# Performance work log

Hardware: AMD Instinct MI355X
Metric: run time of the kernel (lower is better)

The kernel has to match this reference:

```python
import jax, jax.numpy as jnp
import numpy as np


def _conv1x1(x, W, b):
    # x: (n, c_in, h, w); W: (c_out, c_in); b: (c_out,)
    return jnp.einsum('nchw,oc->nohw', x, W) + b[None, :, None, None]


def setup_inputs() -> dict:
    key = jax.random.key(0)
    ks = jax.random.split(key, 9)
    n, C, h, w = 2, 256, 64, 64
    Ch = C // 2
    s_in = 0.02
    return {
        'feature': jax.random.normal(ks[0], (n, C, h, w), dtype=jnp.float32),
        'Wq': jax.random.normal(ks[1], (Ch, C), dtype=jnp.float32) * s_in,
        'bq': jax.random.normal(ks[2], (Ch,), dtype=jnp.float32) * s_in,
        'Wk': jax.random.normal(ks[3], (Ch, C), dtype=jnp.float32) * s_in,
        'bk': jax.random.normal(ks[4], (Ch,), dtype=jnp.float32) * s_in,
        'Wv': jax.random.normal(ks[5], (Ch, C), dtype=jnp.float32) * s_in,
        'bv': jax.random.normal(ks[6], (Ch,), dtype=jnp.float32) * s_in,
        'Wm': jax.random.normal(ks[7], (C, Ch), dtype=jnp.float32) * s_in,
        'bm': jax.random.normal(ks[8], (C,), dtype=jnp.float32) * s_in,
    }


def reference(feature, Wq, bq, Wk, bk, Wv, bv, Wm, bm):
    n, C, h, w = feature.shape
    Ch = C // 2
    N = n * h * w
    # 1x1 conv projections, then flatten batch+spatial into one sequence dim
    q = _conv1x1(feature, Wq, bq)  # (n, Ch, h, w)
    k = _conv1x1(feature, Wk, bk)
    v = _conv1x1(feature, Wv, bv)
    # NCHW -> NHWC -> (N, Ch), matching torch transpose(1,2).transpose(2,3).reshape
    q = jnp.transpose(q, (0, 2, 3, 1)).reshape(N, Ch)
    k = jnp.transpose(k, (0, 2, 3, 1)).reshape(N, Ch)
    v = jnp.transpose(v, (0, 2, 3, 1)).reshape(N, Ch)
    # scores = k @ q.T (note: torch code uses k as rows, q.T as cols)
    scores = k @ q.T  # (N, N)
    attn = jax.nn.softmax(scores, axis=-1)
    mask = attn @ v  # (N, Ch)
    mask = mask.reshape(n, h, w, Ch)
    # torch transpose chain (2,3)->(1,2)->(2,3): (n,h,w,Ch) -> (n,Ch,w,h)
    mask = jnp.transpose(mask, (0, 3, 2, 1))
    out = _conv1x1(mask, Wm, bm)  # (n, C, w, h); h==w so residual add is valid
    return out + feature
```

## Files before the change

kernel.cpp:

```cpp
#include <hip/hip_runtime.h>
#include <hip/hip_bf16.h>

#define LOG2E 1.44269504088896340736f

typedef __attribute__((ext_vector_type(8))) short short8;
typedef __attribute__((ext_vector_type(4))) float f32x4;
typedef __attribute__((ext_vector_type(2))) unsigned int uint2v;
typedef __attribute__((ext_vector_type(4))) unsigned int uint4v;
typedef unsigned int u32;

__device__ __forceinline__ short f2bf(float f) {
    unsigned u = __builtin_bit_cast(unsigned, f);
    unsigned r = (u + 0x7FFFu + ((u >> 16) & 1u)) >> 16;
    return (short)r;
}

__device__ __forceinline__ float bf2f(short x) {
    unsigned u = ((unsigned)(unsigned short)x) << 16;
    return __builtin_bit_cast(float, u);
}

__device__ __forceinline__ unsigned cvt_pk_bf16(float lo, float hi) {
    unsigned r;
    asm volatile("v_cvt_pk_bf16_f32 %0, %1, %2" : "=v"(r) : "v"(lo), "v"(hi));
    return r;
}

__device__ __forceinline__ float fexp2(float x) {
    float r;
    asm("v_exp_f32 %0, %1" : "=v"(r) : "v"(x));
    return r;
}

__global__ __launch_bounds__(64) void wprep_kernel(
    const float* __restrict__ Wq, const float* __restrict__ bq,
    const float* __restrict__ Wk, const float* __restrict__ bk,
    const float* __restrict__ Wv, const float* __restrict__ bv,
    const float* __restrict__ Wm,
    short* __restrict__ Wb, float* __restrict__ bqkv, short* __restrict__ Wmb)
{
    const int b = blockIdx.x;
    const int t = threadIdx.x;
    if (b < 384) {
        const int mat = b >> 7, row = b & 127;
        const float* src = (mat == 0 ? Wq : mat == 1 ? Wk : Wv) + (size_t)row * 256;
        const float sc = (mat == 1) ? LOG2E : 1.f;
        float4 v = *(const float4*)(src + t * 4);
        uint2v pk;
        pk.x = cvt_pk_bf16(v.x * sc, v.y * sc);
        pk.y = cvt_pk_bf16(v.z * sc, v.w * sc);
        *(uint2v*)(Wb + (size_t)b * 256 + t * 4) = pk;
    } else if (b == 384) {
        for (int e = t; e < 384; e += 64) {
            const int mat = e >> 7;
            const float* bsrc = (mat == 0 ? bq : mat == 1 ? bk : bv);
            bqkv[e] = bsrc[e & 127] * (mat == 1 ? LOG2E : 1.f);
        }
    } else {
        const int row = b - 385;
        float2 v = *(const float2*)(Wm + (size_t)row * 128 + t * 2);
        *(u32*)(Wmb + (size_t)row * 128 + t * 2) = cvt_pk_bf16(v.x, v.y);
    }
}

__global__ __launch_bounds__(256) void proj_kernel(
    const float* __restrict__ feat, const short* __restrict__ Wb,
    const float* __restrict__ bqkv,
    short* __restrict__ Qb, short* __restrict__ Kb, short* __restrict__ VTp)
{
    __shared__ __align__(16) short Xs[16 * 256];
    __shared__ __align__(16) short VTs[128 * 16];
    const int t = threadIdx.x;
    const int blk = blockIdx.x;
    const int ib = blk * 16;
    const int n = ib >> 12;
    const int hw0 = ib & 4095;

    {
        const int r = t & 15, cg = t >> 4;
        const float* fp = feat + (size_t)n * 1048576 + (size_t)(cg * 16) * 4096 + hw0 + r;
        short8 t0, t1;
        #pragma unroll
        for (int ci = 0; ci < 8; ++ci) {
            t0[ci] = f2bf(fp[(size_t)ci * 4096]);
            t1[ci] = f2bf(fp[(size_t)(ci + 8) * 4096]);
        }
        const int sw = (r & 7) << 2;
        *(short8*)(&Xs[r * 256 + ((cg * 2) ^ sw) * 8]) = t0;
        *(short8*)(&Xs[r * 256 + ((cg * 2 + 1) ^ sw) * 8]) = t1;
    }
    __syncthreads();

    const int lane = t & 63;
    const int w = __builtin_amdgcn_readfirstlane(t >> 6);
    const int l15 = lane & 15;
    const int g = lane >> 4;
    const int o0w = w * 96;

    f32x4 acc[6];
    #pragma unroll
    for (int osub = 0; osub < 6; ++osub)
        acc[osub] = *(const f32x4*)(bqkv + o0w + osub * 16 + 4 * g);

    const short* wbase = Wb + (size_t)(o0w + l15) * 256 + g * 8;
    const int xsw = (l15 & 7) << 2;
    #pragma unroll
    for (int kc = 0; kc < 8; ++kc) {
        short8 xf = *(const short8*)(&Xs[l15 * 256 + (((kc * 4 + g) ^ xsw) * 8)]);
        #pragma unroll
        for (int osub = 0; osub < 6; ++osub) {
            short8 wf = *(const short8*)(wbase + (size_t)osub * 16 * 256 + kc * 32);
            acc[osub] = __builtin_amdgcn_mfma_f32_16x16x32_bf16(wf, xf, acc[osub], 0, 0, 0);
        }
    }

    #pragma unroll
    for (int osub = 0; osub < 6; ++osub) {
        const int o0 = o0w + osub * 16;
        const int mat = o0 >> 7;
        const int col = (o0 & 127) + 4 * g;
        if (mat == 0) {
            uint2v pk;
            pk.x = cvt_pk_bf16(acc[osub][0], acc[osub][1]);
            pk.y = cvt_pk_bf16(acc[osub][2], acc[osub][3]);
            *(uint2v*)(Qb + (size_t)(ib + l15) * 128 + col) = pk;
        } else if (mat == 1) {
            uint2v pk;
            pk.x = cvt_pk_bf16(acc[osub][0], acc[osub][1]);
            pk.y = cvt_pk_bf16(acc[osub][2], acc[osub][3]);
            *(uint2v*)(Kb + (size_t)(ib + l15) * 128 + col) = pk;
        } else {
            #pragma unroll
            for (int reg = 0; reg < 4; ++reg)
                VTs[(col + reg) * 16 + l15] = f2bf(acc[osub][reg]);
        }
    }
    __syncthreads();

    {
        const int o = t >> 1, ih = (t & 1) * 8;
        short8 vv = *(const short8*)(&VTs[o * 16 + ih]);
        const int base32 = ib & ~31;
        const int u = (ib >> 4) & 1;
        const int p0 = 2 * ih + 4 * u;
        uint4v q = __builtin_bit_cast(uint4v, vv);
        uint2v lo; lo.x = q.x; lo.y = q.y;
        uint2v hi; hi.x = q.z; hi.y = q.w;
        *(uint2v*)(VTp + (size_t)o * 8192 + base32 + p0) = lo;
        *(uint2v*)(VTp + (size_t)o * 8192 + base32 + p0 + 8) = hi;
    }
}

__global__ __launch_bounds__(256, 3) void attn_kernel(
    const short* __restrict__ Qb, const short* __restrict__ Kb,
    const short* __restrict__ VTp,
    short* __restrict__ Opart, float* __restrict__ Ssb)
{
    __shared__ __align__(16) char smem[32768];

    const int tid = threadIdx.x;
    const int lane = tid & 63;
    const int w = __builtin_amdgcn_readfirstlane(tid >> 6);
    const int l15 = lane & 15;
    const int g = lane >> 4;
    const int blk = blockIdx.x;
    const int ibX = blk >> 4;
    const int jq  = blk & 15;
    const int iw  = ibX * 128 + w * 32;
    const int j0  = jq * 512;

    short8 kf[2][4];
    #pragma unroll
    for (int iset = 0; iset < 2; ++iset)
        #pragma unroll
        for (int dcq = 0; dcq < 4; ++dcq)
            kf[iset][dcq] = *(const short8*)(Kb + (size_t)(iw + iset * 16 + l15) * 128 + dcq * 32 + g * 8);

    f32x4 O[2][8];
    #pragma unroll
    for (int iset = 0; iset < 2; ++iset)
        #pragma unroll
        for (int dc = 0; dc < 8; ++dc) O[iset][dc] = (f32x4){0.f, 0.f, 0.f, 0.f};
    float s[2] = {0.f, 0.f};

    auto stage = [&](int tt, int buf) {
        const int jt = j0 + tt * 32;
        char* base = smem + buf * 16384;
        #pragma unroll
        for (int p = 0; p < 4; ++p) {
            const int seg = p * 4 + w;
            const short* src;
            if (seg < 8) {
                int r = 4 * seg + (lane >> 4), c = lane & 15;
                int cs = c ^ (r & 7);
                src = Qb + (size_t)(jt + r) * 128 + cs * 8;
            } else {
                int s8 = seg - 8;
                int d = 16 * s8 + (lane >> 2), c = lane & 3;
                int cs = c ^ (d & 3);
                src = VTp + (size_t)d * 8192 + jt + cs * 8;
            }
            __builtin_amdgcn_global_load_lds(
                (const __attribute__((address_space(1))) u32*)(const void*)src,
                (__attribute__((address_space(3))) u32*)(void*)(base + seg * 1024),
                16, 0, 0);
        }
    };

    auto compute32 = [&](const char* base) {
        const char* Qt = base;
        const char* Vt = base + 8192;
        const int xs = (l15 & 7) << 4;

        f32x4 sv[2][2];
        #pragma unroll
        for (int jh = 0; jh < 2; ++jh)
            #pragma unroll
            for (int iset = 0; iset < 2; ++iset)
                sv[jh][iset] = (f32x4){-16.f, -16.f, -16.f, -16.f};

        __builtin_amdgcn_s_setprio(1);
        #pragma unroll
        for (int dcq = 0; dcq < 4; ++dcq) {
            short8 qa0 = *(const short8*)(Qt + ((l15 * 256 + dcq * 64 + g * 16) ^ xs));
            short8 qa1 = *(const short8*)(Qt + (((l15 + 16) * 256 + dcq * 64 + g * 16) ^ xs));
            sv[0][0] = __builtin_amdgcn_mfma_f32_16x16x32_bf16(qa0, kf[0][dcq], sv[0][0], 0, 0, 0);
            sv[0][1] = __builtin_amdgcn_mfma_f32_16x16x32_bf16(qa0, kf[1][dcq], sv[0][1], 0, 0, 0);
            sv[1][0] = __builtin_amdgcn_mfma_f32_16x16x32_bf16(qa1, kf[0][dcq], sv[1][0], 0, 0, 0);
            sv[1][1] = __builtin_amdgcn_mfma_f32_16x16x32_bf16(qa1, kf[1][dcq], sv[1][1], 0, 0, 0);
        }
        __builtin_amdgcn_s_setprio(0);

        short8 pf[2];
        #pragma unroll
        for (int iset = 0; iset < 2; ++iset) {
            float p0[4], p1[4], ps = 0.f;
            #pragma unroll
            for (int e = 0; e < 4; ++e) {
                p0[e] = fexp2(sv[0][iset][e]);
                p1[e] = fexp2(sv[1][iset][e]);
                ps += p0[e] + p1[e];
            }
            s[iset] += ps;
            uint4v pk;
            pk.x = cvt_pk_bf16(p0[0], p0[1]);
            pk.y = cvt_pk_bf16(p0[2], p0[3]);
            pk.z = cvt_pk_bf16(p1[0], p1[1]);
            pk.w = cvt_pk_bf16(p1[2], p1[3]);
            pf[iset] = __builtin_bit_cast(short8, pk);
        }

        __builtin_amdgcn_s_setprio(1);
        #pragma unroll
        for (int dc = 0; dc < 8; ++dc) {
            short8 va = *(const short8*)(Vt + (dc * 16 + l15) * 64 + ((g ^ (l15 & 3)) << 4));
            O[0][dc] = __builtin_amdgcn_mfma_f32_16x16x32_bf16(va, pf[0], O[0][dc], 0, 0, 0);
            O[1][dc] = __builtin_amdgcn_mfma_f32_16x16x32_bf16(va, pf[1], O[1][dc], 0, 0, 0);
        }
        __builtin_amdgcn_s_setprio(0);
    };

    stage(0, 0);
    __syncthreads();
    int buf = 0;
    for (int tt = 0; tt < 16; ++tt) {
        if (tt + 1 < 16) stage(tt + 1, buf ^ 1);
        compute32(smem + buf * 16384);
        __syncthreads();
        buf ^= 1;
    }

    #pragma unroll
    for (int iset = 0; iset < 2; ++iset) {
        const int i = iw + iset * 16 + l15;
        #pragma unroll
        for (int dc = 0; dc < 8; ++dc) {
            uint2v pk;
            pk.x = cvt_pk_bf16(O[iset][dc][0], O[iset][dc][1]);
            pk.y = cvt_pk_bf16(O[iset][dc][2], O[iset][dc][3]);
            *(uint2v*)(Opart + (size_t)(jq * 8192 + i) * 128 + dc * 16 + 4 * g) = pk;
        }
        Ssb[(((size_t)jq * 8192 + i) << 2) + g] = s[iset];
    }
}

__global__ __launch_bounds__(256) void merge_kernel(
    const short* __restrict__ Opart, const float* __restrict__ Ssb,
    short* __restrict__ maskbb)
{
    const int t = threadIdx.x, b = blockIdx.x;
    const int row = b * 32 + (t >> 3);
    const int d0 = (t & 7) * 16;

    float T = 0.f;
    #pragma unroll
    for (int q = 0; q < 16; ++q) {
        f32x4 s4 = *(const f32x4*)(Ssb + (((size_t)q * 8192 + row) << 2));
        T += (s4[0] + s4[1]) + (s4[2] + s4[3]);
    }

    float acc[16];
    #pragma unroll
    for (int e = 0; e < 16; ++e) acc[e] = 0.f;
    #pragma unroll
    for (int q = 0; q < 16; ++q) {
        const short* op = Opart + (size_t)(q * 8192 + row) * 128 + d0;
        short8 o0 = *(const short8*)(op);
        short8 o1 = *(const short8*)(op + 8);
        #pragma unroll
        for (int e = 0; e < 8; ++e) {
            acc[e]     += bf2f(o0[e]);
            acc[8 + e] += bf2f(o1[e]);
        }
    }
    const float inv = 1.f / T;
    uint4v pk0, pk1;
    pk0.x = cvt_pk_bf16(acc[0] * inv, acc[1] * inv);
    pk0.y = cvt_pk_bf16(acc[2] * inv, acc[3] * inv);
    pk0.z = cvt_pk_bf16(acc[4] * inv, acc[5] * inv);
    pk0.w = cvt_pk_bf16(acc[6] * inv, acc[7] * inv);
    pk1.x = cvt_pk_bf16(acc[8] * inv, acc[9] * inv);
    pk1.y = cvt_pk_bf16(acc[10] * inv, acc[11] * inv);
    pk1.z = cvt_pk_bf16(acc[12] * inv, acc[13] * inv);
    pk1.w = cvt_pk_bf16(acc[14] * inv, acc[15] * inv);
    short* mp = maskbb + (size_t)row * 128 + d0;
    *(uint4v*)(mp) = pk0;
    *(uint4v*)(mp + 8) = pk1;
}

__global__ __launch_bounds__(256, 4) void epi_kernel(
    const short* __restrict__ maskbb, const short* __restrict__ Wmb,
    const float* __restrict__ bm, const float* __restrict__ feat,
    float* __restrict__ out)
{
    __shared__ __align__(16) short Ms[16 * 128];
    const int t = threadIdx.x;
    const int blk = blockIdx.x;
    const int yt = blk & 3;
    const int x = (blk >> 2) & 63;
    const int n = blk >> 8;
    const int y0 = yt * 16;

    {
        const int r = t >> 4, c = t & 15;
        const int i = n * 4096 + (y0 + r) * 64 + x;
        short8 v = *(const short8*)(maskbb + (size_t)i * 128 + c * 8);
        *(short8*)(&Ms[r * 128 + ((c ^ ((r & 7) << 1)) * 8)]) = v;
    }
    __syncthreads();

    const int lane = t & 63;
    const int w = __builtin_amdgcn_readfirstlane(t >> 6);
    const int l15 = lane & 15;
    const int g = lane >> 4;
    const int c0 = w * 64;

    short8 bf[4];
    const int msw = (l15 & 7) << 1;
    #pragma unroll
    for (int dcq = 0; dcq < 4; ++dcq)
        bf[dcq] = *(const short8*)(&Ms[l15 * 128 + (((dcq * 4 + g) ^ msw) * 8)]);

    f32x4 acc[4];
    #pragma unroll
    for (int ct = 0; ct < 4; ++ct)
        acc[ct] = *(const f32x4*)(bm + c0 + ct * 16 + 4 * g);

    const short* wbase = Wmb + (size_t)(c0 + l15) * 128 + g * 8;
    #pragma unroll
    for (int dcq = 0; dcq < 4; ++dcq) {
        #pragma unroll
        for (int ct = 0; ct < 4; ++ct) {
            short8 wf = *(const short8*)(wbase + (size_t)ct * 16 * 128 + dcq * 32);
            acc[ct] = __builtin_amdgcn_mfma_f32_16x16x32_bf16(wf, bf[dcq], acc[ct], 0, 0, 0);
        }
    }

    #pragma unroll
    for (int ct = 0; ct < 4; ++ct) {
        #pragma unroll
        for (int reg = 0; reg < 4; ++reg) {
            const int c = c0 + ct * 16 + 4 * g + reg;
            const size_t oidx = (((size_t)(n * 256 + c) * 64 + x) * 64) + y0 + l15;
            out[oidx] = acc[ct][reg] + feat[oidx];
        }
    }
}

extern "C" void kernel_launch(void* const* d_in, const int* in_sizes, int n_in,
                              void* d_out, int out_size, void* d_ws, size_t ws_size,
                              hipStream_t stream) {
    const float* feat = (const float*)d_in[0];
    const float* Wq = (const float*)d_in[1];
    const float* bq = (const float*)d_in[2];
    const float* Wk = (const float*)d_in[3];
    const float* bk = (const float*)d_in[4];
    const float* Wv = (const float*)d_in[5];
    const float* bv = (const float*)d_in[6];
    const float* Wm = (const float*)d_in[7];
    const float* bm = (const float*)d_in[8];
    float* out = (float*)d_out;

    short* Qb = (short*)d_ws;
    short* Kb = Qb + 8192 * 128;
    short* VTp = Kb + 8192 * 128;
    short* maskbb = VTp + 8192 * 128;
    short* Opart = maskbb + 8192 * 128;
    float* Ssb = (float*)(Opart + (size_t)16 * 8192 * 128);
    float* bqkv = Ssb + (size_t)16 * 8192 * 4;
    short* Wb = (short*)(bqkv + 384);
    short* Wmb = Wb + 384 * 256;

    hipLaunchKernelGGL(wprep_kernel, dim3(641), dim3(64), 0, stream,
                       Wq, bq, Wk, bk, Wv, bv, Wm, Wb, bqkv, Wmb);
    hipLaunchKernelGGL(proj_kernel, dim3(512), dim3(256), 0, stream,
                       feat, Wb, bqkv, Qb, Kb, VTp);
    hipLaunchKernelGGL(attn_kernel, dim3(1024), dim3(256), 0, stream,
                       Qb, Kb, VTp, Opart, Ssb);
    hipLaunchKernelGGL(merge_kernel, dim3(256), dim3(256), 0, stream,
                       Opart, Ssb, maskbb);
    hipLaunchKernelGGL(epi_kernel, dim3(512), dim3(256), 0, stream,
                       maskbb, Wmb, bm, feat, out);
}
```

Baseline: 81.40 us.

## Deepen attention LDS pipeline to four buffers, two tiles per sync

The attention kernel moves from two 16KB LDS buffers to four. It now prefetches two 32-key tiles ahead and computes two tiles between barriers, which halves the number of __syncthreads. Source pointers for the global-to-LDS loads are precomputed once and then advanced by a fixed stride, so the per-stage swizzle address math goes away. The cost is 64KB of LDS per block, and launch bounds drop from 3 to 2 blocks per CU, which lowers occupancy.

New measurement: 81.48 us. About the same (+0.1%).

```diff
diff --git a/kernel.cpp b/kernel.cpp
--- a/kernel.cpp
+++ b/kernel.cpp
@@ -151,12 +151,12 @@
     }
 }
 
-__global__ __launch_bounds__(256, 3) void attn_kernel(
+__global__ __launch_bounds__(256, 2) void attn_kernel(
     const short* __restrict__ Qb, const short* __restrict__ Kb,
     const short* __restrict__ VTp,
     short* __restrict__ Opart, float* __restrict__ Ssb)
 {
-    __shared__ __align__(16) char smem[32768];
+    __shared__ __align__(16) char smem[65536];
 
     const int tid = threadIdx.x;
     const int lane = tid & 63;
@@ -183,28 +183,39 @@
         for (int dc = 0; dc < 8; ++dc) O[iset][dc] = (f32x4){0.f, 0.f, 0.f, 0.f};
     float s[2] = {0.f, 0.f};
 
-    auto stage = [&](int tt, int buf) {
-        const int jt = j0 + tt * 32;
-        char* base = smem + buf * 16384;
-        #pragma unroll
-        for (int p = 0; p < 4; ++p) {
-            const int seg = p * 4 + w;
-            const short* src;
-            if (seg < 8) {
-                int r = 4 * seg + (lane >> 4), c = lane & 15;
-                int cs = c ^ (r & 7);
-                src = Qb + (size_t)(jt + r) * 128 + cs * 8;
-            } else {
-                int s8 = seg - 8;
-                int d = 16 * s8 + (lane >> 2), c = lane & 3;
-                int cs = c ^ (d & 3);
-                src = VTp + (size_t)d * 8192 + jt + cs * 8;
-            }
-            __builtin_amdgcn_global_load_lds(
-                (const __attribute__((address_space(1))) u32*)(const void*)src,
-                (__attribute__((address_space(3))) u32*)(void*)(base + seg * 1024),
-                16, 0, 0);
-        }
+    const short* srcQ0;
+    const short* srcQ1;
+    const short* srcV0;
+    const short* srcV1;
+    {
+        int r0 = 4 * w + (lane >> 4), c0 = lane & 15;
+        srcQ0 = Qb + (size_t)(j0 + r0) * 128 + (c0 ^ (r0 & 7)) * 8;
+        int r1 = 16 + 4 * w + (lane >> 4);
+        srcQ1 = Qb + (size_t)(j0 + r1) * 128 + (c0 ^ (r1 & 7)) * 8;
+        int d0 = 16 * w + (lane >> 2), c2 = lane & 3;
+        srcV0 = VTp + (size_t)d0 * 8192 + j0 + (c2 ^ (d0 & 3)) * 8;
+        int d1 = 64 + 16 * w + (lane >> 2);
+        srcV1 = VTp + (size_t)d1 * 8192 + j0 + (c2 ^ (d1 & 3)) * 8;
+    }
+
+    auto stage = [&](int quarter) {
+        char* base = smem + quarter * 16384;
+        __builtin_amdgcn_global_load_lds(
+            (const __attribute__((address_space(1))) u32*)(const void*)srcQ0,
+            (__attribute__((address_space(3))) u32*)(void*)(base + w * 1024), 16, 0, 0);
+        __builtin_amdgcn_global_load_lds(
+            (const __attribute__((address_space(1))) u32*)(const void*)srcQ1,
+            (__attribute__((address_space(3))) u32*)(void*)(base + (4 + w) * 1024), 16, 0, 0);
+        __builtin_amdgcn_global_load_lds(
+            (const __attribute__((address_space(1))) u32*)(const void*)srcV0,
+            (__attribute__((address_space(3))) u32*)(void*)(base + (8 + w) * 1024), 16, 0, 0);
+        __builtin_amdgcn_global_load_lds(
+            (const __attribute__((address_space(1))) u32*)(const void*)srcV1,
+            (__attribute__((address_space(3))) u32*)(void*)(base + (12 + w) * 1024), 16, 0, 0);
+        srcQ0 += 32 * 128;
+        srcQ1 += 32 * 128;
+        srcV0 += 32;
+        srcV1 += 32;
     };
 
     auto compute32 = [&](const char* base) {
@@ -260,14 +271,17 @@
         __builtin_amdgcn_s_setprio(0);
     };
 
-    stage(0, 0);
+    stage(0);
+    stage(1);
     __syncthreads();
-    int buf = 0;
-    for (int tt = 0; tt < 16; ++tt) {
-        if (tt + 1 < 16) stage(tt + 1, buf ^ 1);
-        compute32(smem + buf * 16384);
+    for (int tt = 0; tt < 16; tt += 2) {
+        if (tt + 2 < 16) {
+            stage((tt + 2) & 3);
+            stage((tt + 3) & 3);
+        }
+        compute32(smem + (tt & 3) * 16384);
+        compute32(smem + ((tt + 1) & 3) * 16384);
         __syncthreads();
-        buf ^= 1;
     }
 
     #pragma unroll
```
